# Kernel tuning notes

Measured on AMD Instinct MI355X. Metric: run time of the kernel, lower is better.

Reference implementation:

```python
import jax, jax.numpy as jnp
import numpy as np

H, D = 16, 64  # heads, head dim; E = H*D


def setup_inputs() -> dict:
    key = jax.random.key(0)
    ks = jax.random.split(key, 8)
    B, T, E = 4, 1024, 1024
    s = (2.0 / E) ** 0.5
    return {
        "x": jax.random.normal(ks[0], (B, T, E), jnp.float32),
        "wq": jax.random.normal(ks[1], (H * D, E), jnp.float32) * s,
        "wk": jax.random.normal(ks[2], (H * D, E), jnp.float32) * s,
        "wv": jax.random.normal(ks[3], (H * D, E), jnp.float32) * s,
        "wvr": jax.random.normal(ks[4], (H * D, E), jnp.float32) * s,
        "wr": jax.random.normal(ks[5], (H, E, T), jnp.float32) * s,
        "wj": jax.random.normal(ks[6], (E, E), jnp.float32) * s,
        "gate": jnp.zeros((H, 3), jnp.float32),
        "wo": jax.random.normal(ks[7], (E, H * D), jnp.float32) * s,
    }


def reference(x, wq, wk, wv, wvr, wr, wj, gate, wo):
    B, T, E = x.shape
    scale = 1.0 / D ** 0.5

    def proj(w):  # torch Linear: y = x @ w.T, then split heads -> (B,H,T,D)
        return jnp.einsum('bte,fe->btf', x, w).reshape(B, T, H, D).transpose(0, 2, 1, 3)

    mask = jnp.triu(jnp.ones((T, T), bool), 1)  # True above diagonal (masked)

    # --- branch 1: standard causal QKV attention ---
    q, k, v = proj(wq), proj(wk), proj(wv)
    s1 = jnp.einsum('bhid,bhjd->bhij', q, k) * scale
    a1 = jax.nn.softmax(jnp.where(mask, -jnp.inf, s1), axis=-1)
    out1 = jnp.einsum('bhij,bhjd->bhid', a1, v)

    # --- branch 2: RRPRAM (parameter-based per-key scores, broadcast over queries) ---
    rv = proj(wvr)
    s2 = jnp.einsum('bte,het->bht', x, wr[:, :, :T]) * scale  # score per key position
    s2 = jnp.broadcast_to(s2[:, :, None, :], (B, H, T, T))
    a2 = jax.nn.softmax(jnp.where(mask, -jnp.inf, s2), axis=-1)
    out2 = jnp.einsum('bhij,bhjd->bhid', a2, rv)

    # --- branch 3: Janus self-echo (rank-1 outer-product scores) ---
    echo = jnp.einsum('bte,fe->btf', x, wj)            # x @ wj.T
    echo_back = jnp.einsum('btf,fe->bte', echo, wj)    # echo @ wj
    sc = jnp.sum(x * echo_back, axis=-1) / (E ** 0.5)  # (B,T)
    s3 = sc[:, :, None] * sc[:, None, :]               # (B,T,T)
    a3 = jax.nn.softmax(jnp.where(mask, -jnp.inf, s3), axis=-1)
    jv = echo.reshape(B, T, H, D).transpose(0, 2, 1, 3)
    out3 = jnp.einsum('bij,bhjd->bhid', a3, jv)

    # --- gated combine (softmax over the 3 branches per head) ---
    g = jax.nn.softmax(gate, axis=-1)  # (H,3)
    out = (g[:, 0][None, :, None, None] * out1
           + g[:, 1][None, :, None, None] * out2
           + g[:, 2][None, :, None, None] * out3)
    out = out.transpose(0, 2, 1, 3).reshape(B, T, H * D)
    return jnp.einsum('btf,ef->bte', out, wo)
```

## Files before the change

### kernel.cpp

```cpp
#include <hip/hip_runtime.h>
#include <cstdint>
#include <cstddef>

typedef unsigned short u16;
typedef short bf16x8 __attribute__((ext_vector_type(8)));
typedef short bf16x4 __attribute__((ext_vector_type(4)));
typedef float f32x4 __attribute__((ext_vector_type(4)));

constexpr int B_ = 4, T_ = 1024, E_ = 1024, H_ = 16, D_ = 64;

__device__ __forceinline__ float bf2f(u16 u) {
  union { unsigned u; float f; } v; v.u = ((unsigned)u) << 16; return v.f;
}
__device__ __forceinline__ u16 f2bf(float f) {
  union { float f; unsigned u; } v; v.f = f;
  return (u16)((v.u + 0x7fffu + ((v.u >> 16) & 1u)) >> 16);
}

#define GLD_LDS16(gp, lp)                                                      \
  __builtin_amdgcn_global_load_lds(                                            \
      (const __attribute__((address_space(1))) void*)(gp),                     \
      (__attribute__((address_space(3))) void*)(lp), 16, 0, 0)

#define SBAR()                                                                 \
  do {                                                                         \
    __builtin_amdgcn_sched_barrier(0);                                         \
    __builtin_amdgcn_s_barrier();                                              \
    __builtin_amdgcn_sched_barrier(0);                                         \
  } while (0)
#define WAIT_LGKM0()                                                           \
  do {                                                                         \
    asm volatile("s_waitcnt lgkmcnt(0)" ::: "memory");                         \
    __builtin_amdgcn_sched_barrier(0);                                         \
  } while (0)
#define WAIT_VM4()                                                             \
  do {                                                                         \
    asm volatile("s_waitcnt vmcnt(4)" ::: "memory");                           \
    __builtin_amdgcn_sched_barrier(0);                                         \
  } while (0)
#define WAIT_VM2()                                                             \
  do {                                                                         \
    asm volatile("s_waitcnt vmcnt(2)" ::: "memory");                           \
    __builtin_amdgcn_sched_barrier(0);                                         \
  } while (0)
#define WAIT_VM0()                                                             \
  do {                                                                         \
    asm volatile("s_waitcnt vmcnt(0)" ::: "memory");                           \
    __builtin_amdgcn_sched_barrier(0);                                         \
  } while (0)

__global__ __launch_bounds__(512, 2) void gemm_qkv8(
    const u16* __restrict__ A, const u16* __restrict__ Bm, u16* __restrict__ C)
{
  __shared__ u16 smem[65536];

  const int tid  = threadIdx.x;
  const int lane = tid & 63;
  const int wave = tid >> 6;
  const int wm = wave >> 2;
  const int wn = wave & 3;
  const int fr = lane & 15;
  const int fg = lane >> 4;
  const int fx = fr & 7;
  const int m0 = blockIdx.y * 256;
  const int n0 = blockIdx.x * 256;

  auto stage = [&](int ktl, int half) {
    const int buf = ktl & 1;
    int kt = (ktl > 15) ? 15 : ktl;
    const int k0 = kt << 6;
    const u16* src = (half < 2)
        ? (A  + (size_t)(m0 + (half & 1) * 128) * 1024)
        : (Bm + (size_t)(n0 + (half & 1) * 128) * 1024);
    u16* dst = smem + (buf << 15) + (half << 13);
    #pragma unroll
    for (int l = 0; l < 2; l++) {
      const int s = (l << 9) | tid;
      const int r = s >> 3, ch = s & 7;
      GLD_LDS16(src + (size_t)r * 1024 + k0 + ((ch ^ (r & 7)) << 3), dst + s * 8);
    }
  };

  f32x4 acc[8][4];
  #pragma unroll
  for (int i = 0; i < 8; i++)
    #pragma unroll
    for (int j = 0; j < 4; j++) acc[i][j] = f32x4{0.f, 0.f, 0.f, 0.f};

  stage(0, 0); stage(0, 1); stage(0, 2); stage(0, 3);
  stage(1, 2); stage(1, 0);
  WAIT_VM4();
  __builtin_amdgcn_s_barrier();
  __builtin_amdgcn_sched_barrier(0);

  const int ko0 = (fg ^ fx) << 3;
  const int ko1 = ((4 | fg) ^ fx) << 3;

  for (int t = 0; t < 16; t++) {
    const int buf = t & 1;
    const int ab = (buf << 15) + (wm << 13) + fr * 64;
    const int bb = (buf << 15) + 16384 + (wn << 12) + fr * 64;

    bf16x8 aF[4][2], bF[4][2];

    #pragma unroll
    for (int mt = 0; mt < 4; mt++) {
      aF[mt][0] = *(const bf16x8*)(smem + ab + mt * 1024 + ko0);
      aF[mt][1] = *(const bf16x8*)(smem + ab + mt * 1024 + ko1);
    }
    #pragma unroll
    for (int nt = 0; nt < 2; nt++) {
      bF[nt][0] = *(const bf16x8*)(smem + bb + nt * 1024 + ko0);
      bF[nt][1] = *(const bf16x8*)(smem + bb + nt * 1024 + ko1);
    }
    stage(t + 1, 1);
    SBAR();
    WAIT_LGKM0();
    __builtin_amdgcn_s_setprio(1);
    #pragma unroll
    for (int mt = 0; mt < 4; mt++)
      #pragma unroll
      for (int nt = 0; nt < 2; nt++) {
        acc[mt][nt] = __builtin_amdgcn_mfma_f32_16x16x32_bf16(aF[mt][0], bF[nt][0], acc[mt][nt], 0, 0, 0);
        acc[mt][nt] = __builtin_amdgcn_mfma_f32_16x16x32_bf16(aF[mt][1], bF[nt][1], acc[mt][nt], 0, 0, 0);
      }
    __builtin_amdgcn_s_setprio(0);
    SBAR();

    #pragma unroll
    for (int nt = 2; nt < 4; nt++) {
      bF[nt][0] = *(const bf16x8*)(smem + bb + nt * 1024 + ko0);
      bF[nt][1] = *(const bf16x8*)(smem + bb + nt * 1024 + ko1);
    }
    stage(t + 1, 3);
    SBAR();
    WAIT_LGKM0();
    __builtin_amdgcn_s_setprio(1);
    #pragma unroll
    for (int mt = 0; mt < 4; mt++)
      #pragma unroll
      for (int nt = 2; nt < 4; nt++) {
        acc[mt][nt] = __builtin_amdgcn_mfma_f32_16x16x32_bf16(aF[mt][0], bF[nt][0], acc[mt][nt], 0, 0, 0);
        acc[mt][nt] = __builtin_amdgcn_mfma_f32_16x16x32_bf16(aF[mt][1], bF[nt][1], acc[mt][nt], 0, 0, 0);
      }
    __builtin_amdgcn_s_setprio(0);
    SBAR();

    #pragma unroll
    for (int mt = 0; mt < 4; mt++) {
      aF[mt][0] = *(const bf16x8*)(smem + ab + (4 + mt) * 1024 + ko0);
      aF[mt][1] = *(const bf16x8*)(smem + ab + (4 + mt) * 1024 + ko1);
    }
    stage(t + 2, 2);
    SBAR();
    WAIT_LGKM0();
    __builtin_amdgcn_s_setprio(1);
    #pragma unroll
    for (int mt = 0; mt < 4; mt++)
      #pragma unroll
      for (int nt = 0; nt < 2; nt++) {
        acc[4 + mt][nt] = __builtin_amdgcn_mfma_f32_16x16x32_bf16(aF[mt][0], bF[nt][0], acc[4 + mt][nt], 0, 0, 0);
        acc[4 + mt][nt] = __builtin_amdgcn_mfma_f32_16x16x32_bf16(aF[mt][1], bF[nt][1], acc[4 + mt][nt], 0, 0, 0);
      }
    __builtin_amdgcn_s_setprio(0);
    SBAR();

    stage(t + 2, 0);
    SBAR();
    __builtin_amdgcn_s_setprio(1);
    #pragma unroll
    for (int mt = 0; mt < 4; mt++)
      #pragma unroll
      for (int nt = 2; nt < 4; nt++) {
        acc[4 + mt][nt] = __builtin_amdgcn_mfma_f32_16x16x32_bf16(aF[mt][0], bF[nt][0], acc[4 + mt][nt], 0, 0, 0);
        acc[4 + mt][nt] = __builtin_amdgcn_mfma_f32_16x16x32_bf16(aF[mt][1], bF[nt][1], acc[4 + mt][nt], 0, 0, 0);
      }
    __builtin_amdgcn_s_setprio(0);
    WAIT_VM4();
    __builtin_amdgcn_s_barrier();
    __builtin_amdgcn_sched_barrier(0);
  }

  u16* Cp = C + (size_t)(m0 + wm * 128) * 4096 + n0 + wn * 64;
  #pragma unroll
  for (int mt = 0; mt < 8; mt++)
    #pragma unroll
    for (int nt = 0; nt < 4; nt++)
      #pragma unroll
      for (int r2 = 0; r2 < 4; r2++)
        Cp[(size_t)(mt * 16 + fg * 4 + r2) * 4096 + nt * 16 + fr] = f2bf(acc[mt][nt][r2]);
}

template<bool CBF16>
__global__ __launch_bounds__(512, 2) void gemm_bt8(
    const u16* __restrict__ A, const u16* __restrict__ Bm, void* __restrict__ Cv,
    int K, int lda, int ldb, int ldc,
    long batchA, long batchB, long batchC, float alpha)
{
  __shared__ u16 smem[32768];

  const int tid  = threadIdx.x;
  const int lane = tid & 63;
  const int wave = tid >> 6;
  const int wm = wave >> 2;
  const int wn = wave & 3;
  const int fr = lane & 15;
  const int fg = lane >> 4;
  const int fx = fr & 7;
  const int m0 = blockIdx.y * 128;
  const int n0 = blockIdx.x * 128;
  const int z  = blockIdx.z;
  const u16* Ab = A  + (size_t)z * batchA;
  const u16* Bb = Bm + (size_t)z * batchB;
  const int NTK = K >> 6;

  auto stage = [&](int ktl, int unit) {
    const int buf = ktl & 1;
    int kt = (ktl > NTK - 1) ? NTK - 1 : ktl;
    const int k0 = kt << 6;
    const u16* src = unit ? (Bb + (size_t)n0 * ldb) : (Ab + (size_t)m0 * lda);
    const int ld = unit ? ldb : lda;
    u16* dst = smem + (buf << 14) + (unit << 13);
    #pragma unroll
    for (int l = 0; l < 2; l++) {
      const int s = (l << 9) | tid;
      const int r = s >> 3, ch = s & 7;
      GLD_LDS16(src + (size_t)r * ld + k0 + ((ch ^ (r & 7)) << 3), dst + s * 8);
    }
  };

  f32x4 acc[4][2];
  #pragma unroll
  for (int i = 0; i < 4; i++)
    #pragma unroll
    for (int j = 0; j < 2; j++) acc[i][j] = f32x4{0.f, 0.f, 0.f, 0.f};

  stage(0, 0); stage(0, 1); stage(1, 0);
  WAIT_VM2();
  __builtin_amdgcn_s_barrier();
  __builtin_amdgcn_sched_barrier(0);

  const int ko0 = (fg ^ fx) << 3;
  const int ko1 = ((4 | fg) ^ fx) << 3;

  for (int t = 0; t < NTK; t++) {
    const int buf = t & 1;
    const int ab = (buf << 14) + (wm * 64 + fr) * 64;
    const int bb = (buf << 14) + 8192 + (wn * 32 + fr) * 64;

    bf16x8 aF[4][2], bF[2];

    #pragma unroll
    for (int mt = 0; mt < 4; mt++) {
      aF[mt][0] = *(const bf16x8*)(smem + ab + mt * 1024 + ko0);
      aF[mt][1] = *(const bf16x8*)(smem + ab + mt * 1024 + ko1);
    }
    bF[0] = *(const bf16x8*)(smem + bb + ko0);
    bF[1] = *(const bf16x8*)(smem + bb + ko1);
    stage(t + 1, 1);
    SBAR();
    WAIT_LGKM0();
    __builtin_amdgcn_s_setprio(1);
    #pragma unroll
    for (int mt = 0; mt < 4; mt++) {
      acc[mt][0] = __builtin_amdgcn_mfma_f32_16x16x32_bf16(aF[mt][0], bF[0], acc[mt][0], 0, 0, 0);
      acc[mt][0] = __builtin_amdgcn_mfma_f32_16x16x32_bf16(aF[mt][1], bF[1], acc[mt][0], 0, 0, 0);
    }
    __builtin_amdgcn_s_setprio(0);
    SBAR();

    bF[0] = *(const bf16x8*)(smem + bb + 1024 + ko0);
    bF[1] = *(const bf16x8*)(smem + bb + 1024 + ko1);
    stage(t + 2, 0);
    SBAR();
    WAIT_LGKM0();
    __builtin_amdgcn_s_setprio(1);
    #pragma unroll
    for (int mt = 0; mt < 4; mt++) {
      acc[mt][1] = __builtin_amdgcn_mfma_f32_16x16x32_bf16(aF[mt][0], bF[0], acc[mt][1], 0, 0, 0);
      acc[mt][1] = __builtin_amdgcn_mfma_f32_16x16x32_bf16(aF[mt][1], bF[1], acc[mt][1], 0, 0, 0);
    }
    __builtin_amdgcn_s_setprio(0);
    WAIT_VM2();
    __builtin_amdgcn_s_barrier();
    __builtin_amdgcn_sched_barrier(0);
  }

  WAIT_VM0();
  #pragma unroll
  for (int mt = 0; mt < 4; mt++) {
    #pragma unroll
    for (int nt = 0; nt < 2; nt++) {
      const int row = m0 + wm * 64 + mt * 16 + fg * 4;
      const int col = n0 + wn * 32 + nt * 16 + fr;
      #pragma unroll
      for (int r2 = 0; r2 < 4; r2++) {
        const float vv = acc[mt][nt][r2] * alpha;
        const size_t ci = (size_t)z * batchC + (size_t)(row + r2) * ldc + col;
        if constexpr (CBF16) ((u16*)Cv)[ci] = f2bf(vv);
        else                 ((float*)Cv)[ci] = vv;
      }
    }
  }
}

__global__ __launch_bounds__(512, 2) void gemm_echo8(
    const u16* __restrict__ A, const u16* __restrict__ Alo,
    const u16* __restrict__ Bm, const u16* __restrict__ Blo,
    u16* __restrict__ echoT, float* __restrict__ sc)
{
  __shared__ u16 smem[65536];

  const int tid  = threadIdx.x;
  const int lane = tid & 63;
  const int wave = tid >> 6;
  const int wm = wave >> 2;
  const int wn = wave & 3;
  const int fr = lane & 15;
  const int fg = lane >> 4;
  const int fx = fr & 7;
  const int m0 = blockIdx.y * 128;
  const int n0 = blockIdx.x * 128;

  auto stage = [&](int ktl, int unit) {
    const int buf = ktl & 1;
    int kt = (ktl > 15) ? 15 : ktl;
    const int k0 = kt << 6;
    const u16* src = (unit == 0) ? A   + (size_t)m0 * 1024
                   : (unit == 1) ? Alo + (size_t)m0 * 1024
                   : (unit == 2) ? Bm  + (size_t)n0 * 1024
                   :               Blo + (size_t)n0 * 1024;
    u16* dst = smem + (buf << 15) + (unit << 13);
    #pragma unroll
    for (int l = 0; l < 2; l++) {
      const int s = (l << 9) | tid;
      const int r = s >> 3, ch = s & 7;
      GLD_LDS16(src + (size_t)r * 1024 + k0 + ((ch ^ (r & 7)) << 3), dst + s * 8);
    }
  };

  f32x4 acc[4][2];
  #pragma unroll
  for (int i = 0; i < 4; i++)
    #pragma unroll
    for (int j = 0; j < 2; j++) acc[i][j] = f32x4{0.f, 0.f, 0.f, 0.f};

  stage(0, 0); stage(0, 1); stage(0, 2); stage(0, 3);
  stage(1, 0); stage(1, 1);
  WAIT_VM4();
  __builtin_amdgcn_s_barrier();
  __builtin_amdgcn_sched_barrier(0);

  const int ko0 = (fg ^ fx) << 3;
  const int ko1 = ((4 | fg) ^ fx) << 3;

  for (int t = 0; t < 16; t++) {
    const int buf = t & 1;
    const int ab = (buf << 15) + (wm * 64 + fr) * 64;
    const int bb = (buf << 15) + 16384 + (wn * 32 + fr) * 64;

    bf16x8 aH[4][2], aL[4][2], bH[2], bL[2];

    #pragma unroll
    for (int mt = 0; mt < 4; mt++) {
      aH[mt][0] = *(const bf16x8*)(smem + ab + mt * 1024 + ko0);
      aH[mt][1] = *(const bf16x8*)(smem + ab + mt * 1024 + ko1);
      aL[mt][0] = *(const bf16x8*)(smem + ab + 8192 + mt * 1024 + ko0);
      aL[mt][1] = *(const bf16x8*)(smem + ab + 8192 + mt * 1024 + ko1);
    }
    bH[0] = *(const bf16x8*)(smem + bb + ko0);
    bL[0] = *(const bf16x8*)(smem + bb + 8192 + ko0);
    bH[1] = *(const bf16x8*)(smem + bb + ko1);
    bL[1] = *(const bf16x8*)(smem + bb + 8192 + ko1);
    stage(t + 1, 2);
    stage(t + 1, 3);
    SBAR();
    WAIT_LGKM0();
    __builtin_amdgcn_s_setprio(1);
    #pragma unroll
    for (int mt = 0; mt < 4; mt++) {
      acc[mt][0] = __builtin_amdgcn_mfma_f32_16x16x32_bf16(aH[mt][0], bH[0], acc[mt][0], 0, 0, 0);
      acc[mt][0] = __builtin_amdgcn_mfma_f32_16x16x32_bf16(aL[mt][0], bH[0], acc[mt][0], 0, 0, 0);
      acc[mt][0] = __builtin_amdgcn_mfma_f32_16x16x32_bf16(aH[mt][0], bL[0], acc[mt][0], 0, 0, 0);
    }
    #pragma unroll
    for (int mt = 0; mt < 4; mt++) {
      acc[mt][0] = __builtin_amdgcn_mfma_f32_16x16x32_bf16(aH[mt][1], bH[1], acc[mt][0], 0, 0, 0);
      acc[mt][0] = __builtin_amdgcn_mfma_f32_16x16x32_bf16(aL[mt][1], bH[1], acc[mt][0], 0, 0, 0);
      acc[mt][0] = __builtin_amdgcn_mfma_f32_16x16x32_bf16(aH[mt][1], bL[1], acc[mt][0], 0, 0, 0);
    }
    __builtin_amdgcn_s_setprio(0);
    SBAR();

    bH[0] = *(const bf16x8*)(smem + bb + 1024 + ko0);
    bL[0] = *(const bf16x8*)(smem + bb + 8192 + 1024 + ko0);
    bH[1] = *(const bf16x8*)(smem + bb + 1024 + ko1);
    bL[1] = *(const bf16x8*)(smem + bb + 8192 + 1024 + ko1);
    stage(t + 2, 0);
    stage(t + 2, 1);
    SBAR();
    WAIT_LGKM0();
    __builtin_amdgcn_s_setprio(1);
    #pragma unroll
    for (int mt = 0; mt < 4; mt++) {
      acc[mt][1] = __builtin_amdgcn_mfma_f32_16x16x32_bf16(aH[mt][0], bH[0], acc[mt][1], 0, 0, 0);
      acc[mt][1] = __builtin_amdgcn_mfma_f32_16x16x32_bf16(aL[mt][0], bH[0], acc[mt][1], 0, 0, 0);
      acc[mt][1] = __builtin_amdgcn_mfma_f32_16x16x32_bf16(aH[mt][0], bL[0], acc[mt][1], 0, 0, 0);
    }
    #pragma unroll
    for (int mt = 0; mt < 4; mt++) {
      acc[mt][1] = __builtin_amdgcn_mfma_f32_16x16x32_bf16(aH[mt][1], bH[1], acc[mt][1], 0, 0, 0);
      acc[mt][1] = __builtin_amdgcn_mfma_f32_16x16x32_bf16(aL[mt][1], bH[1], acc[mt][1], 0, 0, 0);
      acc[mt][1] = __builtin_amdgcn_mfma_f32_16x16x32_bf16(aH[mt][1], bL[1], acc[mt][1], 0, 0, 0);
    }
    __builtin_amdgcn_s_setprio(0);
    WAIT_VM4();
    __builtin_amdgcn_s_barrier();
    __builtin_amdgcn_sched_barrier(0);
  }

  asm volatile("s_waitcnt vmcnt(0) lgkmcnt(0)" ::: "memory");
  __builtin_amdgcn_sched_barrier(0);
  __builtin_amdgcn_s_barrier();
  __builtin_amdgcn_sched_barrier(0);

  const int b   = m0 >> 10;
  const int t0l = m0 & 1023;
  u16* lt = smem;

  #pragma unroll
  for (int mt = 0; mt < 4; mt++) {
    float sq[4] = {0.f, 0.f, 0.f, 0.f};
    #pragma unroll
    for (int nt = 0; nt < 2; nt++) {
      const int cl = wn * 32 + nt * 16 + fr;
      #pragma unroll
      for (int r2 = 0; r2 < 4; r2++) {
        const float vv = acc[mt][nt][r2];
        sq[r2] += vv * vv;
        lt[cl * 132 + wm * 64 + mt * 16 + fg * 4 + r2] = f2bf(vv);
      }
    }
    #pragma unroll
    for (int m2 = 1; m2 < 16; m2 <<= 1) {
      sq[0] += __shfl_xor(sq[0], m2, 64);
      sq[1] += __shfl_xor(sq[1], m2, 64);
      sq[2] += __shfl_xor(sq[2], m2, 64);
      sq[3] += __shfl_xor(sq[3], m2, 64);
    }
    if (fr == 0) {
      #pragma unroll
      for (int r2 = 0; r2 < 4; r2++)
        atomicAdd(&sc[(size_t)b * T_ + t0l + wm * 64 + mt * 16 + fg * 4 + r2], sq[r2]);
    }
  }
  __syncthreads();
  for (int s = tid; s < 128 * 128; s += 512) {
    const int f = s >> 7, tt = s & 127;
    echoT[((size_t)b * E_ + n0 + f) * T_ + t0l + tt] = lt[f * 132 + tt];
  }
}

__global__ __launch_bounds__(256, 4) void flash1p2(
    const u16* __restrict__ qkvr, const u16* __restrict__ vTb,
    const u16* __restrict__ out2, const u16* __restrict__ out3,
    const float* __restrict__ gate, u16* __restrict__ comb) {
  const int x = blockIdx.x, h = blockIdx.y, b = blockIdx.z;
  const int tid = threadIdx.x, lane = tid & 63, w = tid >> 6;
  const int fr = lane & 15, fg = lane >> 4;
  const int itA = x, itB = 15 - x;

  __shared__ u16 sQ[4096];
  __shared__ u16 sK[2][8192];
  __shared__ u16 sV[2][8192];

  const u16* Kb = qkvr + (size_t)(b * T_) * 4096 + 1024 + h * 64;
  const u16* Vb = vTb + (size_t)(b * H_ + h) * (D_ * T_);

  const float g0 = gate[h * 3 + 0], g1 = gate[h * 3 + 1], g2 = gate[h * 3 + 2];
  const float gmx = fmaxf(g0, fmaxf(g1, g2));
  const float e0 = __expf(g0 - gmx), e1 = __expf(g1 - gmx), e2 = __expf(g2 - gmx);
  const float ginv = 1.0f / (e0 + e1 + e2);

  auto stageQ = [&](int it) {
    const u16* Qb = qkvr + ((size_t)(b * T_) + it * 64) * 4096 + h * 64;
    #pragma unroll
    for (int s0 = 0; s0 < 512; s0 += 256) {
      const int s = s0 + tid;
      const int l = s & 63, g = s >> 6;
      const int row = (g >> 1) * 16 + (l & 15);
      const int c8  = (g & 1) * 4 + (l >> 4);
      GLD_LDS16(Qb + (size_t)row * 4096 + c8 * 8, &sQ[s * 8]);
    }
  };
  auto stageKV = [&](int jt, int bi) {
    #pragma unroll
    for (int s0 = 0; s0 < 1024; s0 += 256) {
      const int s = s0 + tid;
      const int l = s & 63, g = s >> 6;
      const int row = (g >> 1) * 16 + (l & 15);
      const int c8  = (g & 1) * 4 + (l >> 4);
      GLD_LDS16(Kb + (size_t)(jt * 128 + row) * 4096 + c8 * 8, &sK[bi][s * 8]);
    }
    #pragma unroll
    for (int s0 = 0; s0 < 1024; s0 += 256) {
      const int s = s0 + tid;
      const int jc = s >> 6, d = s & 63;
      GLD_LDS16(Vb + ((size_t)(jt * 16 + jc)) * 512 + d * 8, &sV[bi][s * 8]);
    }
  };

  stageQ(itA);
  stageKV(0, 0);
  asm volatile("s_waitcnt vmcnt(0)" ::: "memory");
  __syncthreads();

  bf16x8 bQ[2];
  f32x4 accO[4];
  float mrow, lrow;
  int cnt = 0;

  #pragma unroll 1
  for (int ph = 0; ph < 2; ph++) {
    const int it = ph ? itB : itA;
    const int nsteps = (it >> 1) + 1;

    #pragma unroll
    for (int kk = 0; kk < 2; kk++)
      bQ[kk] = *(const bf16x8*)&sQ[(((w * 2 + kk) << 6) | lane) * 8];
    mrow = -3.0e38f; lrow = 0.f;
    #pragma unroll
    for (int nd = 0; nd < 4; nd++) accO[nd] = f32x4{0.f, 0.f, 0.f, 0.f};

    for (int jt = 0; jt < nsteps; jt++, cnt++) {
      const int bi = cnt & 1;

      if (jt < nsteps - 1) {
        stageKV(jt + 1, bi ^ 1);
      } else if (ph == 0) {
        stageQ(itB);
        stageKV(0, bi ^ 1);
      }

      f32x4 accST[8];
      #pragma unroll
      for (int nf = 0; nf < 8; nf++) accST[nf] = f32x4{0.f, 0.f, 0.f, 0.f};
      #pragma unroll
      for (int kk = 0; kk < 2; kk++) {
        #pragma unroll
        for (int nf = 0; nf < 8; nf++) {
          const bf16x8 aK = *(const bf16x8*)&sK[bi][((((nf << 1) | kk) << 6) | lane) * 8];
          accST[nf] = __builtin_amdgcn_mfma_f32_16x16x32_bf16(aK, bQ[kk], accST[nf], 0, 0, 0);
        }
      }

      const bool diag = (jt == nsteps - 1);
      const int iloc = it * 64 + w * 16 + fr;
      float sv[8][4];
      float rmax = -3.0e38f;
      #pragma unroll
      for (int nf = 0; nf < 8; nf++)
        #pragma unroll
        for (int r = 0; r < 4; r++) {
          float s = accST[nf][r] * 0.125f;
          if (diag && (jt * 128 + nf * 16 + fg * 4 + r) > iloc) s = -3.0e38f;
          sv[nf][r] = s;
          rmax = fmaxf(rmax, s);
        }
      rmax = fmaxf(rmax, __shfl_xor(rmax, 16, 64));
      rmax = fmaxf(rmax, __shfl_xor(rmax, 32, 64));
      const float mn = fmaxf(mrow, rmax);
      const float al = __expf(mrow - mn);
      mrow = mn;
      float ps = 0.f;
      bf16x4 pf[8];
      #pragma unroll
      for (int nf = 0; nf < 8; nf++)
        #pragma unroll
        for (int r = 0; r < 4; r++) {
          const float pv = __expf(sv[nf][r] - mn);
          ps += pv;
          pf[nf][r] = (short)f2bf(pv);
        }
      ps += __shfl_xor(ps, 16, 64);
      ps += __shfl_xor(ps, 32, 64);
      lrow = lrow * al + ps;
      #pragma unroll
      for (int r = 0; r < 4; r++) {
        const float alr = __shfl(al, fg * 4 + r, 64);
        #pragma unroll
        for (int nd = 0; nd < 4; nd++) accO[nd][r] *= alr;
      }

      #pragma unroll
      for (int kc = 0; kc < 8; kc++) {
        bf16x8 bV[4];
        #pragma unroll
        for (int nd = 0; nd < 4; nd++) {
          const bf16x4 vv = *(const bf16x4*)&sV[bi][
              (((kc * 2 + (fg >> 1)) * 64 + nd * 16 + fr) * 8) + (fg & 1) * 4];
          bV[nd] = bf16x8{vv[0], vv[1], vv[2], vv[3], 0, 0, 0, 0};
        }
        const bf16x4 pp = pf[kc];
        const bf16x8 pA = bf16x8{pp[0], pp[1], pp[2], pp[3], 0, 0, 0, 0};
        #pragma unroll
        for (int nd = 0; nd < 4; nd++)
          accO[nd] = __builtin_amdgcn_mfma_f32_16x16x32_bf16(pA, bV[nd], accO[nd], 0, 0, 0);
      }

      asm volatile("s_waitcnt vmcnt(0)" ::: "memory");
      __syncthreads();
    }

    const int bfree = (cnt + 1) & 1;
    u16* lt = &sK[bfree][0];
    const float li = 1.0f / lrow;
    #pragma unroll
    for (int r = 0; r < 4; r++) {
      const float linv = __shfl(li, fg * 4 + r, 64);
      const int row = w * 16 + fg * 4 + r;
      #pragma unroll
      for (int nd = 0; nd < 4; nd++)
        lt[row * 72 + nd * 16 + fr] = f2bf(accO[nd][r] * linv);
    }
    __syncthreads();
    const size_t rbase = ((size_t)(b * T_) + it * 64) * E_ + h * 64;
    #pragma unroll
    for (int s0 = 0; s0 < 512; s0 += 256) {
      const int s = s0 + tid;
      const int row = s >> 3, c8 = (s & 7) * 8;
      const size_t gidx = rbase + (size_t)row * E_ + c8;
      const bf16x8 o1v = *(const bf16x8*)&lt[row * 72 + c8];
      const bf16x8 o2v = *(const bf16x8*)&out2[gidx];
      const bf16x8 o3v = *(const bf16x8*)&out3[gidx];
      bf16x8 ov;
      #pragma unroll
      for (int e = 0; e < 8; e++) {
        const float o = (e0 * bf2f((u16)o1v[e]) + e1 * bf2f((u16)o2v[e])
                       + e2 * bf2f((u16)o3v[e])) * ginv;
        ov[e] = (short)f2bf(o);
      }
      *(bf16x8*)&comb[gidx] = ov;
    }
    __syncthreads();
  }
}

__device__ __forceinline__ float block_max256(float v, float* red) {
  #pragma unroll
  for (int m = 32; m > 0; m >>= 1) v = fmaxf(v, __shfl_xor(v, m, 64));
  if ((threadIdx.x & 63) == 0) red[threadIdx.x >> 6] = v;
  __syncthreads();
  const float r = fmaxf(fmaxf(red[0], red[1]), fmaxf(red[2], red[3]));
  __syncthreads();
  return r;
}
__device__ __forceinline__ float block_sum256(float v, float* red) {
  #pragma unroll
  for (int m = 32; m > 0; m >>= 1) v += __shfl_xor(v, m, 64);
  if ((threadIdx.x & 63) == 0) red[threadIdx.x >> 6] = v;
  __syncthreads();
  const float r = (red[0] + red[1]) + (red[2] + red[3]);
  __syncthreads();
  return r;
}

__global__ __launch_bounds__(256) void cast_all(
    const float* __restrict__ x, const float* __restrict__ wq,
    const float* __restrict__ wk, const float* __restrict__ wv,
    const float* __restrict__ wvr, const float* __restrict__ wo,
    const float* __restrict__ wj,
    u16* __restrict__ xb, u16* __restrict__ xlo, u16* __restrict__ wcat,
    u16* __restrict__ wob, u16* __restrict__ wjb, u16* __restrict__ wjlo) {
  const int bid = blockIdx.x;
  if (bid < 4096) {
    const size_t i = ((size_t)bid * 256 + threadIdx.x) * 4;
    const float4 v = *(const float4*)(x + i);
    ushort4 oh, ol;
    oh.x = f2bf(v.x); ol.x = f2bf(v.x - bf2f(oh.x));
    oh.y = f2bf(v.y); ol.y = f2bf(v.y - bf2f(oh.y));
    oh.z = f2bf(v.z); ol.z = f2bf(v.z - bf2f(oh.z));
    oh.w = f2bf(v.w); ol.w = f2bf(v.w - bf2f(oh.w));
    *(ushort4*)(xb + i) = oh;
    *(ushort4*)(xlo + i) = ol;
  } else if (bid < 8192) {
    const int r = (bid - 4096) >> 10;
    const float* src = (r == 0) ? wq : (r == 1) ? wk : (r == 2) ? wv : wvr;
    const size_t i = ((size_t)((bid - 4096) & 1023) * 256 + threadIdx.x) * 4;
    const float4 v = *(const float4*)(src + i);
    ushort4 o;
    o.x = f2bf(v.x); o.y = f2bf(v.y); o.z = f2bf(v.z); o.w = f2bf(v.w);
    *(ushort4*)(wcat + (size_t)r * (1 << 20) + i) = o;
  } else if (bid < 9216) {
    const size_t i = ((size_t)(bid - 8192) * 256 + threadIdx.x) * 4;
    const float4 v = *(const float4*)(wo + i);
    ushort4 o;
    o.x = f2bf(v.x); o.y = f2bf(v.y); o.z = f2bf(v.z); o.w = f2bf(v.w);
    *(ushort4*)(wob + i) = o;
  } else {
    const size_t i = ((size_t)(bid - 9216) * 256 + threadIdx.x) * 4;
    const float4 v = *(const float4*)(wj + i);
    ushort4 oh, ol;
    oh.x = f2bf(v.x); ol.x = f2bf(v.x - bf2f(oh.x));
    oh.y = f2bf(v.y); ol.y = f2bf(v.y - bf2f(oh.y));
    oh.z = f2bf(v.z); ol.z = f2bf(v.z - bf2f(oh.z));
    oh.w = f2bf(v.w); ol.w = f2bf(v.w - bf2f(oh.w));
    *(ushort4*)(wjb + i) = oh;
    *(ushort4*)(wjlo + i) = ol;
  }
}

__global__ __launch_bounds__(256) void s2_direct(
    const u16* __restrict__ xb, const float* __restrict__ wr, float* __restrict__ s2) {
  const int t0 = blockIdx.x * 32, h = blockIdx.y;
  const int tt = threadIdx.x & 31, eg = threadIdx.x >> 5;
  float acc[4] = {0.f, 0.f, 0.f, 0.f};
  const float* wp = wr + (size_t)h * E_ * T_ + t0 + tt;
  for (int ec = 0; ec < 8; ec++) {
    const int e0 = ec * 128 + eg * 16;
    bf16x8 xv[4][2];
    #pragma unroll
    for (int b = 0; b < 4; b++) {
      const u16* xp = xb + ((size_t)(b * T_) + t0 + tt) * E_ + e0;
      xv[b][0] = *(const bf16x8*)xp;
      xv[b][1] = *(const bf16x8*)(xp + 8);
    }
    #pragma unroll
    for (int e2 = 0; e2 < 16; e2++) {
      const float w = wp[(size_t)(e0 + e2) * T_];
      #pragma unroll
      for (int b = 0; b < 4; b++)
        acc[b] += bf2f((u16)xv[b][e2 >> 3][e2 & 7]) * w;
    }
  }
  __shared__ float red[8][4][33];
  #pragma unroll
  for (int b = 0; b < 4; b++) red[eg][b][tt] = acc[b];
  __syncthreads();
  if (threadIdx.x < 128) {
    const int b = threadIdx.x >> 5, t = threadIdx.x & 31;
    float s = 0.f;
    #pragma unroll
    for (int g = 0; g < 8; g++) s += red[g][b][t];
    s2[((size_t)b * H_ + h) * T_ + t0 + t] = s * 0.125f;
  }
}

__global__ __launch_bounds__(256) void a3_softmax(const float* __restrict__ sc, u16* __restrict__ a3) {
  const int i = blockIdx.x;
  const int b = blockIdx.y;
  const float* sr = sc + (size_t)b * T_;
  const float sci = sr[i] * 0.03125f;
  u16* row = a3 + ((size_t)b * T_ + i) * T_;
  __shared__ float red[4];
  float v[4];
  float m = -3.0e38f;
  #pragma unroll
  for (int k = 0; k < 4; k++) {
    const int j = threadIdx.x + k * 256;
    const float xv = (j <= i) ? sci * (sr[j] * 0.03125f) : -3.0e38f;
    v[k] = xv;
    m = fmaxf(m, xv);
  }
  m = block_max256(m, red);
  float s = 0.f;
  #pragma unroll
  for (int k = 0; k < 4; k++) {
    const int j = threadIdx.x + k * 256;
    const float p = (j <= i) ? __expf(v[k] - m) : 0.f;
    v[k] = p;
    s += p;
  }
  s = block_sum256(s, red);
  const float inv = 1.0f / s;
  #pragma unroll
  for (int k = 0; k < 4; k++) {
    const int j = threadIdx.x + k * 256;
    row[j] = f2bf(v[k] * inv);
  }
}

__global__ __launch_bounds__(1024) void branch2_scan(
    const float* __restrict__ s2, const u16* __restrict__ rv, int ldrv,
    u16* __restrict__ out2) {
  const int h = blockIdx.x, b = blockIdx.y;
  const int tid = threadIdx.x;
  const int lane = tid & 63;
  const int wv = tid >> 6;

  const float* srow = s2 + ((size_t)b * H_ + h) * T_;

  __shared__ float wbuf[T_];
  __shared__ float numtot[16][64];
  __shared__ float dentot[16];
  __shared__ float redm[16];

  float m = srow[tid];
  #pragma unroll
  for (int mk = 32; mk > 0; mk >>= 1) m = fmaxf(m, __shfl_xor(m, mk, 64));
  if (lane == 0) redm[wv] = m;
  __syncthreads();
  m = redm[0];
  #pragma unroll
  for (int i2 = 1; i2 < 16; i2++) m = fmaxf(m, redm[i2]);

  wbuf[tid] = __expf(srow[tid] - m);
  __syncthreads();

  const u16* rvp = rv + (size_t)(b * T_) * ldrv + h * D_ + lane;
  const int j0 = wv * 64;
  float num = 0.f, den = 0.f;
  #pragma unroll 8
  for (int j2 = 0; j2 < 64; j2++) {
    const float w = wbuf[j0 + j2];
    den += w;
    num += w * bf2f(rvp[(size_t)(j0 + j2) * ldrv]);
  }
  numtot[wv][lane] = num;
  if (lane == 0) dentot[wv] = den;
  __syncthreads();

  float num_off = 0.f, den_off = 0.f;
  for (int w2 = 0; w2 < wv; w2++) {
    num_off += numtot[w2][lane];
    den_off += dentot[w2];
  }

  u16* op = out2 + (size_t)b * T_ * E_ + h * D_ + lane;
  num = num_off; den = den_off;
  #pragma unroll 8
  for (int j2 = 0; j2 < 64; j2++) {
    const float w = wbuf[j0 + j2];
    num += w * bf2f(rvp[(size_t)(j0 + j2) * ldrv]);
    den += w;
    op[(size_t)(j0 + j2) * E_] = f2bf(num / den);
  }
}

__global__ __launch_bounds__(256) void transpose_v(const u16* __restrict__ v, u16* __restrict__ vTb,
                                                   int ldv) {
  const int bh = blockIdx.x;
  const int b = bh >> 4, h = bh & 15;
  const int d0 = blockIdx.y * 32, t0 = blockIdx.z * 32;
  __shared__ u16 tile[32][33];
  const int c = threadIdx.x & 31, r0 = threadIdx.x >> 5;
  #pragma unroll
  for (int rr = 0; rr < 32; rr += 8) {
    const int t = t0 + rr + r0;
    tile[rr + r0][c] = v[((size_t)b * T_ + t) * ldv + h * 64 + d0 + c];
  }
  __syncthreads();
  #pragma unroll
  for (int rr = 0; rr < 32; rr += 8) {
    const int d = d0 + rr + r0;
    const int t = t0 + c;
    vTb[((size_t)(bh * 128 + (t >> 3)) * 64 + d) * 8 + (t & 7)] = tile[c][rr + r0];
  }
}

extern "C" void kernel_launch(void* const* d_in, const int* in_sizes, int n_in,
                              void* d_out, int out_size, void* d_ws, size_t ws_size,
                              hipStream_t stream) {
  (void)in_sizes; (void)n_in; (void)out_size; (void)ws_size;
  const float* x    = (const float*)d_in[0];
  const float* wq   = (const float*)d_in[1];
  const float* wk   = (const float*)d_in[2];
  const float* wv   = (const float*)d_in[3];
  const float* wvr  = (const float*)d_in[4];
  const float* wr   = (const float*)d_in[5];
  const float* wj   = (const float*)d_in[6];
  const float* gate = (const float*)d_in[7];
  const float* wo   = (const float*)d_in[8];
  float* out = (float*)d_out;

  char* p = (char*)d_ws;
  auto alloc = [&](size_t bytes) -> char* {
    char* r = p; p += (bytes + 255) & ~(size_t)255; return r;
  };
  const size_t NTE = (size_t)B_ * T_ * E_;
  const size_t NW  = (size_t)E_ * E_;

  u16* xb    = (u16*)alloc(NTE * 2);
  u16* xlo   = (u16*)alloc(NTE * 2);
  u16* wcat  = (u16*)alloc(4 * NW * 2);
  u16* wjb   = (u16*)alloc(NW * 2);
  u16* wjlo  = (u16*)alloc(NW * 2);
  u16* wob   = (u16*)alloc(NW * 2);
  u16* qkvr  = (u16*)alloc(NTE * 4 * 2);
  u16* vT    = (u16*)alloc(NTE * 2);
  u16* echoT = (u16*)alloc(NTE * 2);
  u16* a3p   = (u16*)alloc(NTE * 2);
  float* sc  = (float*)alloc((size_t)B_ * T_ * 4);
  float* s2  = (float*)alloc((size_t)B_ * H_ * T_ * 4);
  u16* out2b = (u16*)alloc(NTE * 2);
  u16* out3b = (u16*)alloc(NTE * 2);
  u16* comb  = (u16*)alloc(NTE * 2);

  cast_all<<<dim3(10240), 256, 0, stream>>>(x, wq, wk, wv, wvr, wo, wj,
                                            xb, xlo, wcat, wob, wjb, wjlo);
  hipMemsetAsync(sc, 0, (size_t)B_ * T_ * 4, stream);

  gemm_qkv8<<<dim3(16, 16), 512, 0, stream>>>(xb, wcat, qkvr);

  gemm_echo8<<<dim3(8, 32), 512, 0, stream>>>(xb, xlo, wjb, wjlo, echoT, sc);

  transpose_v<<<dim3(B_ * H_, D_ / 32, T_ / 32), 256, 0, stream>>>(qkvr + 2048, vT, 4096);
  s2_direct<<<dim3(T_ / 32, H_), 256, 0, stream>>>(xb, wr, s2);

  branch2_scan<<<dim3(H_, B_), 1024, 0, stream>>>(s2, qkvr + 3072, 4096, out2b);

  a3_softmax<<<dim3(T_, B_), 256, 0, stream>>>(sc, a3p);
  gemm_bt8<true><<<dim3(E_ / 128, T_ / 128, B_), 512, 0, stream>>>(
      a3p, echoT, out3b, T_, T_, T_, E_,
      (long)T_ * T_, (long)E_ * T_, (long)T_ * E_, 1.f);

  flash1p2<<<dim3(8, H_, B_), 256, 0, stream>>>(qkvr, vT, out2b, out3b, gate, comb);

  gemm_bt8<false><<<dim3(E_ / 128, (B_ * T_) / 128, 1), 512, 0, stream>>>(
      comb, wob, out, E_, E_, E_, E_, 0L, 0L, 0L, 1.f);
}
```

Baseline: 330.3 us.

## Process paired causal query tiles jointly sharing each K/V stage

The flash attention kernel used to run its two paired query tiles (itA and 15-itA) one after the other, loading K/V separately for each. It now keeps both tiles' Q fragments and accumulators live and walks the K/V tiles once, applying each loaded tile to both queries while the short tile is still active. This cuts redundant K/V global loads and LDS staging and interleaves independent MFMA chains. In exchange, register pressure roughly doubles, and launch bounds drop from 4 to 2 blocks per CU, which may lower occupancy.

```diff
diff --git a/kernel.cpp b/kernel.cpp
--- a/kernel.cpp
+++ b/kernel.cpp
@@ -461,7 +461,7 @@
   }
 }
 
-__global__ __launch_bounds__(256, 4) void flash1p2(
+__global__ __launch_bounds__(256, 2) void flash1q(
     const u16* __restrict__ qkvr, const u16* __restrict__ vTb,
     const u16* __restrict__ out2, const u16* __restrict__ out3,
     const float* __restrict__ gate, u16* __restrict__ comb) {
@@ -469,8 +469,9 @@
   const int tid = threadIdx.x, lane = tid & 63, w = tid >> 6;
   const int fr = lane & 15, fg = lane >> 4;
   const int itA = x, itB = 15 - x;
-
-  __shared__ u16 sQ[4096];
+  const int nA = (itA >> 1) + 1, nB = (itB >> 1) + 1;
+
+  __shared__ u16 sQ[2][4096];
   __shared__ u16 sK[2][8192];
   __shared__ u16 sV[2][8192];
 
@@ -482,7 +483,7 @@
   const float e0 = __expf(g0 - gmx), e1 = __expf(g1 - gmx), e2 = __expf(g2 - gmx);
   const float ginv = 1.0f / (e0 + e1 + e2);
 
-  auto stageQ = [&](int it) {
+  auto stageQ = [&](int it, int qb) {
     const u16* Qb = qkvr + ((size_t)(b * T_) + it * 64) * 4096 + h * 64;
     #pragma unroll
     for (int s0 = 0; s0 < 512; s0 += 256) {
@@ -490,7 +491,7 @@
       const int l = s & 63, g = s >> 6;
       const int row = (g >> 1) * 16 + (l & 15);
       const int c8  = (g & 1) * 4 + (l >> 4);
-      GLD_LDS16(Qb + (size_t)row * 4096 + c8 * 8, &sQ[s * 8]);
+      GLD_LDS16(Qb + (size_t)row * 4096 + c8 * 8, &sQ[qb][s * 8]);
     }
   };
   auto stageKV = [&](int jt, int bi) {
@@ -510,88 +511,101 @@
     }
   };
 
-  stageQ(itA);
+  auto sm_step = [&](f32x4 (&st)[8], int it, int kbase, bool diag,
+                     float& mrow, float& lrow, f32x4 (&accO)[4], bf16x4 (&pf)[8]) {
+    const int iloc = it * 64 + w * 16 + fr;
+    float sv[8][4];
+    float rmax = -3.0e38f;
+    #pragma unroll
+    for (int nf = 0; nf < 8; nf++)
+      #pragma unroll
+      for (int r = 0; r < 4; r++) {
+        float s = st[nf][r] * 0.125f;
+        if (diag && (kbase + nf * 16 + fg * 4 + r) > iloc) s = -3.0e38f;
+        sv[nf][r] = s;
+        rmax = fmaxf(rmax, s);
+      }
+    rmax = fmaxf(rmax, __shfl_xor(rmax, 16, 64));
+    rmax = fmaxf(rmax, __shfl_xor(rmax, 32, 64));
+    const float mn = fmaxf(mrow, rmax);
+    const float al = __expf(mrow - mn);
+    mrow = mn;
+    float ps = 0.f;
+    #pragma unroll
+    for (int nf = 0; nf < 8; nf++)
+      #pragma unroll
+      for (int r = 0; r < 4; r++) {
+        const float pv = __expf(sv[nf][r] - mn);
+        ps += pv;
+        pf[nf][r] = (short)f2bf(pv);
+      }
+    ps += __shfl_xor(ps, 16, 64);
+    ps += __shfl_xor(ps, 32, 64);
+    lrow = lrow * al + ps;
+    #pragma unroll
+    for (int r = 0; r < 4; r++) {
+      const float alr = __shfl(al, fg * 4 + r, 64);
+      #pragma unroll
+      for (int nd = 0; nd < 4; nd++) accO[nd][r] *= alr;
+    }
+  };
+
+  stageQ(itA, 0);
+  stageQ(itB, 1);
   stageKV(0, 0);
   asm volatile("s_waitcnt vmcnt(0)" ::: "memory");
   __syncthreads();
 
-  bf16x8 bQ[2];
-  f32x4 accO[4];
-  float mrow, lrow;
-  int cnt = 0;
-
-  #pragma unroll 1
-  for (int ph = 0; ph < 2; ph++) {
-    const int it = ph ? itB : itA;
-    const int nsteps = (it >> 1) + 1;
-
-    #pragma unroll
-    for (int kk = 0; kk < 2; kk++)
-      bQ[kk] = *(const bf16x8*)&sQ[(((w * 2 + kk) << 6) | lane) * 8];
-    mrow = -3.0e38f; lrow = 0.f;
-    #pragma unroll
-    for (int nd = 0; nd < 4; nd++) accO[nd] = f32x4{0.f, 0.f, 0.f, 0.f};
-
-    for (int jt = 0; jt < nsteps; jt++, cnt++) {
-      const int bi = cnt & 1;
-
-      if (jt < nsteps - 1) {
-        stageKV(jt + 1, bi ^ 1);
-      } else if (ph == 0) {
-        stageQ(itB);
-        stageKV(0, bi ^ 1);
-      }
-
-      f32x4 accST[8];
-      #pragma unroll
-      for (int nf = 0; nf < 8; nf++) accST[nf] = f32x4{0.f, 0.f, 0.f, 0.f};
-      #pragma unroll
-      for (int kk = 0; kk < 2; kk++) {
+  bf16x8 bQA[2], bQB[2];
+  #pragma unroll
+  for (int kk = 0; kk < 2; kk++) {
+    bQA[kk] = *(const bf16x8*)&sQ[0][(((w * 2 + kk) << 6) | lane) * 8];
+    bQB[kk] = *(const bf16x8*)&sQ[1][(((w * 2 + kk) << 6) | lane) * 8];
+  }
+
+  f32x4 accOA[4], accOB[4];
+  float mA = -3.0e38f, lA = 0.f, mB = -3.0e38f, lB = 0.f;
+  #pragma unroll
+  for (int nd = 0; nd < 4; nd++) {
+    accOA[nd] = f32x4{0.f, 0.f, 0.f, 0.f};
+    accOB[nd] = f32x4{0.f, 0.f, 0.f, 0.f};
+  }
+
+  for (int jt = 0; jt < nB; jt++) {
+    const int bi = jt & 1;
+    if (jt < nB - 1) stageKV(jt + 1, bi ^ 1);
+    const bool actA = (jt < nA);
+
+    f32x4 stA[8], stB[8];
+    #pragma unroll
+    for (int nf = 0; nf < 8; nf++) {
+      stA[nf] = f32x4{0.f, 0.f, 0.f, 0.f};
+      stB[nf] = f32x4{0.f, 0.f, 0.f, 0.f};
+    }
+    if (actA) {
+      #pragma unroll
+      for (int kk = 0; kk < 2; kk++)
         #pragma unroll
         for (int nf = 0; nf < 8; nf++) {
           const bf16x8 aK = *(const bf16x8*)&sK[bi][((((nf << 1) | kk) << 6) | lane) * 8];
-          accST[nf] = __builtin_amdgcn_mfma_f32_16x16x32_bf16(aK, bQ[kk], accST[nf], 0, 0, 0);
+          stB[nf] = __builtin_amdgcn_mfma_f32_16x16x32_bf16(aK, bQB[kk], stB[nf], 0, 0, 0);
+          stA[nf] = __builtin_amdgcn_mfma_f32_16x16x32_bf16(aK, bQA[kk], stA[nf], 0, 0, 0);
         }
-      }
-
-      const bool diag = (jt == nsteps - 1);
-      const int iloc = it * 64 + w * 16 + fr;
-      float sv[8][4];
-      float rmax = -3.0e38f;
-      #pragma unroll
-      for (int nf = 0; nf < 8; nf++)
+    } else {
+      #pragma unroll
+      for (int kk = 0; kk < 2; kk++)
         #pragma unroll
-        for (int r = 0; r < 4; r++) {
-          float s = accST[nf][r] * 0.125f;
-          if (diag && (jt * 128 + nf * 16 + fg * 4 + r) > iloc) s = -3.0e38f;
-          sv[nf][r] = s;
-          rmax = fmaxf(rmax, s);
+        for (int nf = 0; nf < 8; nf++) {
+          const bf16x8 aK = *(const bf16x8*)&sK[bi][((((nf << 1) | kk) << 6) | lane) * 8];
+          stB[nf] = __builtin_amdgcn_mfma_f32_16x16x32_bf16(aK, bQB[kk], stB[nf], 0, 0, 0);
         }
-      rmax = fmaxf(rmax, __shfl_xor(rmax, 16, 64));
-      rmax = fmaxf(rmax, __shfl_xor(rmax, 32, 64));
-      const float mn = fmaxf(mrow, rmax);
-      const float al = __expf(mrow - mn);
-      mrow = mn;
-      float ps = 0.f;
-      bf16x4 pf[8];
-      #pragma unroll
-      for (int nf = 0; nf < 8; nf++)
-        #pragma unroll
-        for (int r = 0; r < 4; r++) {
-          const float pv = __expf(sv[nf][r] - mn);
-          ps += pv;
-          pf[nf][r] = (short)f2bf(pv);
-        }
-      ps += __shfl_xor(ps, 16, 64);
-      ps += __shfl_xor(ps, 32, 64);
-      lrow = lrow * al + ps;
-      #pragma unroll
-      for (int r = 0; r < 4; r++) {
-        const float alr = __shfl(al, fg * 4 + r, 64);
-        #pragma unroll
-        for (int nd = 0; nd < 4; nd++) accO[nd][r] *= alr;
-      }
-
+    }
+
+    bf16x4 pfA[8], pfB[8];
+    sm_step(stB, itB, jt * 128, jt == nB - 1, mB, lB, accOB, pfB);
+    if (actA) sm_step(stA, itA, jt * 128, jt == nA - 1, mA, lA, accOA, pfA);
+
+    if (actA) {
       #pragma unroll
       for (int kc = 0; kc < 8; kc++) {
         bf16x8 bV[4];
@@ -601,48 +615,74 @@
               (((kc * 2 + (fg >> 1)) * 64 + nd * 16 + fr) * 8) + (fg & 1) * 4];
           bV[nd] = bf16x8{vv[0], vv[1], vv[2], vv[3], 0, 0, 0, 0};
         }
-        const bf16x4 pp = pf[kc];
-        const bf16x8 pA = bf16x8{pp[0], pp[1], pp[2], pp[3], 0, 0, 0, 0};
+        const bf16x4 pb = pfB[kc];
+        const bf16x8 pB = bf16x8{pb[0], pb[1], pb[2], pb[3], 0, 0, 0, 0};
+        const bf16x4 pa = pfA[kc];
+        const bf16x8 pA = bf16x8{pa[0], pa[1], pa[2], pa[3], 0, 0, 0, 0};
+        #pragma unroll
+        for (int nd = 0; nd < 4; nd++) {
+          accOB[nd] = __builtin_amdgcn_mfma_f32_16x16x32_bf16(pB, bV[nd], accOB[nd], 0, 0, 0);
+          accOA[nd] = __builtin_amdgcn_mfma_f32_16x16x32_bf16(pA, bV[nd], accOA[nd], 0, 0, 0);
+        }
+      }
+    } else {
+      #pragma unroll
+      for (int kc = 0; kc < 8; kc++) {
+        bf16x8 bV[4];
+        #pragma unroll
+        for (int nd = 0; nd < 4; nd++) {
+          const bf16x4 vv = *(const bf16x4*)&sV[bi][
+              (((kc * 2 + (fg >> 1)) * 64 + nd * 16 + fr) * 8) + (fg & 1) * 4];
+          bV[nd] = bf16x8{vv[0], vv[1], vv[2], vv[3], 0, 0, 0, 0};
+        }
+        const bf16x4 pb = pfB[kc];
+        const bf16x8 pB = bf16x8{pb[0], pb[1], pb[2], pb[3], 0, 0, 0, 0};
         #pragma unroll
         for (int nd = 0; nd < 4; nd++)
-          accO[nd] = __builtin_amdgcn_mfma_f32_16x16x32_bf16(pA, bV[nd], accO[nd], 0, 0, 0);
+          accOB[nd] = __builtin_amdgcn_mfma_f32_16x16x32_bf16(pB, bV[nd], accOB[nd], 0, 0, 0);
       }
-
-      asm volatile("s_waitcnt vmcnt(0)" ::: "memory");
-      __syncthreads();
-    }
-
-    const int bfree = (cnt + 1) & 1;
-    u16* lt = &sK[bfree][0];
-    const float li = 1.0f / lrow;
-    #pragma unroll
-    for (int r = 0; r < 4; r++) {
-      const float linv = __shfl(li, fg * 4 + r, 64);
-      const int row = w * 16 + fg * 4 + r;
-      #pragma unroll
-      for (int nd = 0; nd < 4; nd++)
-        lt[row * 72 + nd * 16 + fr] = f2bf(accO[nd][r] * linv);
-    }
+    }
+
+    asm volatile("s_waitcnt vmcnt(0)" ::: "memory");
     __syncthreads();
-    const size_t rbase = ((size_t)(b * T_) + it * 64) * E_ + h * 64;
-    #pragma unroll
-    for (int s0 = 0; s0 < 512; s0 += 256) {
-      const int s = s0 + tid;
-      const int row = s >> 3, c8 = (s & 7) * 8;
-      const size_t gidx = rbase + (size_t)row * E_ + c8;
-      const bf16x8 o1v = *(const bf16x8*)&lt[row * 72 + c8];
-      const bf16x8 o2v = *(const bf16x8*)&out2[gidx];
-      const bf16x8 o3v = *(const bf16x8*)&out3[gidx];
-      bf16x8 ov;
-      #pragma unroll
-      for (int e = 0; e < 8; e++) {
-        const float o = (e0 * bf2f((u16)o1v[e]) + e1 * bf2f((u16)o2v[e])
-                       + e2 * bf2f((u16)o3v[e])) * ginv;
-        ov[e] = (short)f2bf(o);
-      }
-      *(bf16x8*)&comb[gidx] = ov;
-    }
-    __syncthreads();
+  }
+
+  u16* ltA = &sK[0][0];
+  u16* ltB = &sK[1][0];
+  const float liA = 1.0f / lA;
+  const float liB = 1.0f / lB;
+  #pragma unroll
+  for (int r = 0; r < 4; r++) {
+    const float lvA = __shfl(liA, fg * 4 + r, 64);
+    const float lvB = __shfl(liB, fg * 4 + r, 64);
+    const int row = w * 16 + fg * 4 + r;
+    #pragma unroll
+    for (int nd = 0; nd < 4; nd++) {
+      ltA[row * 72 + nd * 16 + fr] = f2bf(accOA[nd][r] * lvA);
+      ltB[row * 72 + nd * 16 + fr] = f2bf(accOB[nd][r] * lvB);
+    }
+  }
+  __syncthreads();
+  #pragma unroll
+  for (int s0 = 0; s0 < 1024; s0 += 256) {
+    const int s = s0 + tid;
+    const int tile = s >> 9;
+    const int sr = s & 511;
+    const int row = sr >> 3, c8 = (sr & 7) * 8;
+    const int it = tile ? itB : itA;
+    const u16* lt = tile ? ltB : ltA;
+    const size_t gidx = ((size_t)(b * T_) + it * 64 + row) * E_ + h * 64 + c8;
+    const bf16x8 o1v = *(const bf16x8*)&lt[row * 72 + c8];
+    const bf16x8 o2v = *(const bf16x8*)&out2[gidx];
+    const bf16x8 o3v = *(const bf16x8*)&out3[gidx];
+    bf16x8 ov;
+    #pragma unroll
+    for (int e = 0; e < 8; e++) {
+      const float o = (e0 * bf2f((u16)o1v[e]) + e1 * bf2f((u16)o2v[e])
+                     + e2 * bf2f((u16)o3v[e])) * ginv;
+      ov[e] = (short)f2bf(o);
+    }
+    *(bf16x8*)&comb[gidx] = ov;
   }
 }
 
@@ -914,7 +954,7 @@
       a3p, echoT, out3b, T_, T_, T_, E_,
       (long)T_ * T_, (long)E_ * T_, (long)T_ * E_, 1.f);
 
-  flash1p2<<<dim3(8, H_, B_), 256, 0, stream>>>(qkvr, vT, out2b, out3b, gate, comb);
+  flash1q<<<dim3(8, H_, B_), 256, 0, stream>>>(qkvr, vT, out2b, out3b, gate, comb);
 
   gemm_bt8<false><<<dim3(E_ / 128, (B_ * T_) / 128, 1), 512, 0, stream>>>(
       comb, wob, out, E_, E_, E_, E_, 0L, 0L, 0L, 1.f);
```

After: 328.2 us. About the same (-0.6%).
